# Kernel optimization log

Measured on AMD Instinct MI355X. Metric: run time of the kernel, lower is better.

## Reference

```python
import jax, jax.numpy as jnp
import numpy as np

B, T, S, H, L = 64, 512, 400, 768, 9


def setup_inputs() -> dict:
    rng = np.random.default_rng(0)
    attn = np.zeros((B, T), np.int32)
    ids_lens = np.zeros((B, S), np.int32)
    for bi in range(B):
        Lb = int(rng.integers(T // 2, T + 1))  # valid wordpiece count
        lens = []
        rem = Lb
        while rem > 0 and len(lens) < S - 1:
            l = int(min(rng.integers(1, 4), rem))  # 1-3 wordpieces per word
            lens.append(l)
            rem -= l
        if rem > 0:
            lens.append(rem)
        attn[bi, :Lb] = 1
        ids_lens[bi, :len(lens)] = np.asarray(lens, np.int32)
    label_ids = rng.integers(0, L, (B, S)).astype(np.int32)
    label_mask = ids_lens > 0
    key = jax.random.key(0)
    k1, k2 = jax.random.split(key)
    last_enc_out = jax.random.normal(k1, (B, T, H), jnp.float32)
    W = jax.random.normal(k2, (H, L), jnp.float32) * 0.02
    b = jnp.zeros((L,), jnp.float32)
    return {
        'last_enc_out': last_enc_out, 'W': W, 'b': b,
        'attention_mask': jnp.asarray(attn), 'ids_lens': jnp.asarray(ids_lens),
        'label_ids': jnp.asarray(label_ids), 'label_mask': jnp.asarray(label_mask),
    }


def reference(last_enc_out, W, b, attention_mask, ids_lens, label_ids, label_mask):
    Bv, Tv, Hv = last_enc_out.shape
    Sv = ids_lens.shape[1]
    # position of each valid token among the row's valid tokens
    tok_pos = jnp.cumsum(attention_mask, axis=1) - 1            # [B,T]
    cum = jnp.cumsum(ids_lens, axis=1)                          # [B,S] nondecreasing
    # word index for each token: first w with cum[w] > tok_pos
    word_idx = jax.vmap(lambda c, p: jnp.searchsorted(c, p, side='right'))(cum, tok_pos)
    valid = attention_mask > 0
    seg = jnp.where(valid, jnp.arange(Bv)[:, None] * Sv + word_idx, Bv * Sv)  # dump slot for pad
    sums = jax.ops.segment_sum(last_enc_out.reshape(Bv * Tv, Hv), seg.reshape(Bv * Tv),
                               num_segments=Bv * Sv + 1)[:Bv * Sv]
    counts = jnp.maximum(ids_lens.reshape(Bv * Sv), 1).astype(last_enc_out.dtype)
    means = (sums / counts[:, None]).reshape(Bv, Sv, Hv)
    word_mask = ids_lens > 0
    bert_embed = jnp.where(word_mask[:, :, None], means, jnp.zeros((), last_enc_out.dtype))
    # dropout is identity in eval mode
    logits = bert_embed @ W + b                                 # [B,S,L]
    logp = jax.nn.log_softmax(logits, axis=-1)
    nll = -jnp.take_along_axis(logp, label_ids[..., None].astype(jnp.int32), axis=-1)[..., 0]
    mf = label_mask.astype(logits.dtype)
    loss = jnp.sum(nll * mf) / jnp.sum(mf)                      # CE with ignore_index masking
    output = jnp.argmax(logits, axis=-1)
    return loss, output
```

## Files before the change

### kernel.cpp

```cpp
#include <hip/hip_runtime.h>
#include <math.h>

#define Bdim 64
#define Tdim 512
#define Sdim 400
#define Hdim 768
#define Ldim 9
#define PSTRIDE 12

#define PROJ_BLOCKS 2048
#define ROWS_PER_BLK 16

template <int CTRL>
__device__ __forceinline__ float dpp_add(float x) {
  int y = __builtin_amdgcn_update_dpp(0, __float_as_int(x), CTRL, 0xF, 0xF, false);
  return x + __int_as_float(y);
}
__device__ __forceinline__ float wave_sum63(float x) {
  x = dpp_add<0x111>(x);
  x = dpp_add<0x112>(x);
  x = dpp_add<0x114>(x);
  x = dpp_add<0x118>(x);
  x = dpp_add<0x142>(x);
  x = dpp_add<0x143>(x);
  return x;
}

__global__ __launch_bounds__(192, 4) void proj_kernel(
    const float* __restrict__ enc, const float* __restrict__ W,
    float* __restrict__ proj, float* __restrict__ accum,
    unsigned* __restrict__ counter) {
  int tid = threadIdx.x;
  int lane = tid & 63;
  int w = tid >> 6;
  int l0 = w * 3;
  int base = blockIdx.x * ROWS_PER_BLK;

  if (blockIdx.x == 0) {
    if (tid < 2) accum[tid] = 0.0f;
    if (tid == 2) *counter = 0u;
  }

  float wf[3][4][3];
#pragma unroll
  for (int k = 0; k < 3; ++k)
#pragma unroll
    for (int j = 0; j < 4; ++j) {
      int h = 4 * lane + 256 * k + j;
#pragma unroll
      for (int c = 0; c < 3; ++c) wf[k][j][c] = W[(size_t)h * Ldim + l0 + c];
    }

  const float4* encf4 = (const float4*)enc;

  float4 xa0, xa1, xa2, xb0, xb1, xb2;
#define LDROW(v0, v1, v2, IDX)                                             \
  {                                                                        \
    const float4* r_ = encf4 + (size_t)(base + (IDX)) * (Hdim / 4);        \
    v0 = r_[lane]; v1 = r_[lane + 64]; v2 = r_[lane + 128];                \
  }
#define PROCROW(v0, v1, v2, IDX)                                           \
  {                                                                        \
    float dd[3];                                                           \
    _Pragma("unroll") for (int c = 0; c < 3; ++c) {                        \
      dd[c] = v0.x * wf[0][0][c] + v0.y * wf[0][1][c] +                    \
              v0.z * wf[0][2][c] + v0.w * wf[0][3][c] +                    \
              v1.x * wf[1][0][c] + v1.y * wf[1][1][c] +                    \
              v1.z * wf[1][2][c] + v1.w * wf[1][3][c] +                    \
              v2.x * wf[2][0][c] + v2.y * wf[2][1][c] +                    \
              v2.z * wf[2][2][c] + v2.w * wf[2][3][c];                     \
      dd[c] = wave_sum63(dd[c]);                                           \
    }                                                                      \
    if (lane == 63) {                                                      \
      float* dst = proj + (size_t)(base + (IDX)) * PSTRIDE + l0;           \
      dst[0] = dd[0]; dst[1] = dd[1]; dst[2] = dd[2];                      \
    }                                                                      \
  }

  LDROW(xa0, xa1, xa2, 0)
  LDROW(xb0, xb1, xb2, 1)
#pragma unroll
  for (int i = 0; i < ROWS_PER_BLK; i += 2) {
    PROCROW(xa0, xa1, xa2, i)
    if (i + 2 < ROWS_PER_BLK) LDROW(xa0, xa1, xa2, i + 2)
    PROCROW(xb0, xb1, xb2, i + 1)
    if (i + 3 < ROWS_PER_BLK) LDROW(xb0, xb1, xb2, i + 3)
  }
#undef LDROW
#undef PROCROW
}

__global__ __launch_bounds__(Tdim) void rowword_kernel(
    const float* __restrict__ proj, const float* __restrict__ bias,
    const int* __restrict__ attn, const int* __restrict__ ids_lens,
    const int* __restrict__ label_ids, float* __restrict__ out,
    float* __restrict__ accum, unsigned* __restrict__ counter) {
  int b = blockIdx.x;
  int tid = threadIdx.x;
  int lane = tid & 63, wid = tid >> 6;
  __shared__ int p2t[Tdim];
  __shared__ int wst[Sdim];
  __shared__ int wsum[8];
  __shared__ int totsm;
  __shared__ float ssm[8], csm[8];

  int m = attn[b * Tdim + tid];
  int x = m;
#pragma unroll
  for (int off = 1; off < 64; off <<= 1) {
    int v = __shfl_up(x, off, 64);
    if (lane >= off) x += v;
  }
  if (lane == 63) wsum[wid] = x;
  __syncthreads();
  if (tid < 8) {
    int s = wsum[tid], y = s;
#pragma unroll
    for (int off = 1; off < 8; off <<= 1) {
      int v = __shfl_up(y, off, 64);
      if (tid >= off) y += v;
    }
    wsum[tid] = y - s;
    if (tid == 7) totsm = y;
  }
  __syncthreads();
  x += wsum[wid];
  if (m) p2t[x - 1] = tid;
  int nv_local = totsm;
  __syncthreads();

  int len = (tid < Sdim) ? ids_lens[b * Sdim + tid] : 0;
  int x2 = len;
#pragma unroll
  for (int off = 1; off < 64; off <<= 1) {
    int v = __shfl_up(x2, off, 64);
    if (lane >= off) x2 += v;
  }
  if (lane == 63) wsum[wid] = x2;
  __syncthreads();
  if (tid < 8) {
    int s = wsum[tid], y = s;
#pragma unroll
    for (int off = 1; off < 8; off <<= 1) {
      int v = __shfl_up(y, off, 64);
      if (tid >= off) y += v;
    }
    wsum[tid] = y - s;
  }
  __syncthreads();
  x2 += wsum[wid];
  if (tid < Sdim) wst[tid] = x2 - len;
  __syncthreads();

  float nll = 0.0f, cnt = 0.0f;
  if (tid < Sdim) {
    int bs = b * Sdim + tid;
    float sum[Ldim];
#pragma unroll
    for (int l = 0; l < Ldim; ++l) sum[l] = 0.0f;
    if (len > 0) {
      int start = wst[tid];
      for (int j = 0; j < len; ++j) {
        int q = start + j;
        if (q >= nv_local) break;
        const float* pr = proj + ((size_t)(b << 9) + p2t[q]) * PSTRIDE;
        const float4* pr4 = (const float4*)pr;
        float4 r0 = pr4[0], r1 = pr4[1];
        float r8 = pr[8];
        sum[0] += r0.x; sum[1] += r0.y; sum[2] += r0.z; sum[3] += r0.w;
        sum[4] += r1.x; sum[5] += r1.y; sum[6] += r1.z; sum[7] += r1.w;
        sum[8] += r8;
      }
    }
    float inv = (len > 0) ? 1.0f / (float)len : 0.0f;
    float lg[Ldim];
#pragma unroll
    for (int l = 0; l < Ldim; ++l) lg[l] = sum[l] * inv + bias[l];

    int amax = 0;
    float mx = lg[0];
#pragma unroll
    for (int l = 1; l < Ldim; ++l)
      if (lg[l] > mx) { mx = lg[l]; amax = l; }
    out[1 + bs] = (float)amax;

    if (len > 0) {
      float se = 0.0f;
#pragma unroll
      for (int l = 0; l < Ldim; ++l) se += expf(lg[l] - mx);
      float lse = mx + logf(se);
      int lab = label_ids[bs];
      float ll = lg[0];
#pragma unroll
      for (int l = 1; l < Ldim; ++l) ll = (lab == l) ? lg[l] : ll;
      nll = lse - ll;
      cnt = 1.0f;
    }
  }

#pragma unroll
  for (int off = 32; off > 0; off >>= 1) {
    nll += __shfl_down(nll, off, 64);
    cnt += __shfl_down(cnt, off, 64);
  }
  if (lane == 0) { ssm[wid] = nll; csm[wid] = cnt; }
  __syncthreads();
  if (tid == 0) {
    float S = 0.f, C = 0.f;
#pragma unroll
    for (int k = 0; k < 8; ++k) { S += ssm[k]; C += csm[k]; }
    atomicAdd(&accum[0], S);
    atomicAdd(&accum[1], C);
    __threadfence();
    unsigned prev = atomicAdd(counter, 1u);
    if (prev == gridDim.x - 1) {
      __threadfence();
      float Sf = atomicAdd(&accum[0], 0.0f);
      float Cf = atomicAdd(&accum[1], 0.0f);
      out[0] = Sf / Cf;
    }
  }
}

extern "C" void kernel_launch(void* const* d_in, const int* in_sizes, int n_in,
                              void* d_out, int out_size, void* d_ws, size_t ws_size,
                              hipStream_t stream) {
  const float* enc     = (const float*)d_in[0];
  const float* W       = (const float*)d_in[1];
  const float* bias    = (const float*)d_in[2];
  const int* attn      = (const int*)d_in[3];
  const int* ids_lens  = (const int*)d_in[4];
  const int* label_ids = (const int*)d_in[5];

  float* out = (float*)d_out;

  char* ws = (char*)d_ws;
  size_t off0 = 0;
  float* accum      = (float*)(ws + off0);    off0 += 128;
  unsigned* counter = (unsigned*)(ws + off0); off0 += 128;
  float* proj       = (float*)(ws + off0);    off0 += (size_t)Bdim * Tdim * PSTRIDE * sizeof(float);

  proj_kernel<<<PROJ_BLOCKS, 192, 0, stream>>>(enc, W, proj, accum, counter);
  rowword_kernel<<<Bdim, Tdim, 0, stream>>>(proj, bias, attn, ids_lens,
                                            label_ids, out, accum, counter);
}
```

Baseline: 34.58 us.

## Fuse projection and word pooling per batch quarter, skip padded tokens

Combines the token projection and the per-word pooling/loss into a single kernel that launches four blocks per batch row. Each block compacts the valid tokens, projects only a window of them (its 128-token quarter plus a small overlap) into shared memory, and pools the words that start in that quarter. This removes the global proj buffer round-trip and skips projecting padded tokens. The atomic counter finalisation is replaced by per-block partials and a tiny reduction kernel. In exchange, the grid is only 256 blocks of 512 threads, so the projection has less parallelism than the 2048-block version. Overlap tokens are also projected twice.

```diff
diff --git a/kernel.cpp b/kernel.cpp
--- a/kernel.cpp
+++ b/kernel.cpp
@@ -6,10 +6,9 @@
 #define Sdim 400
 #define Hdim 768
 #define Ldim 9
-#define PSTRIDE 12
-
-#define PROJ_BLOCKS 2048
-#define ROWS_PER_BLK 16
+
+#define QWIN 130
+#define LPROJ_ROWS 132
 
 template <int CTRL>
 __device__ __forceinline__ float dpp_add(float x) {
@@ -26,175 +25,178 @@
   return x;
 }
 
-__global__ __launch_bounds__(192, 4) void proj_kernel(
+__global__ __launch_bounds__(512, 2) void fused_kernel(
     const float* __restrict__ enc, const float* __restrict__ W,
-    float* __restrict__ proj, float* __restrict__ accum,
-    unsigned* __restrict__ counter) {
+    const float* __restrict__ bias, const int* __restrict__ attn,
+    const int* __restrict__ ids_lens, const int* __restrict__ label_ids,
+    float* __restrict__ out, float2* __restrict__ partials) {
+  int blk = blockIdx.x;
+  int b = blk >> 2;
+  int part = blk & 3;
+  int q0 = part << 7;
   int tid = threadIdx.x;
-  int lane = tid & 63;
-  int w = tid >> 6;
-  int l0 = w * 3;
-  int base = blockIdx.x * ROWS_PER_BLK;
-
-  if (blockIdx.x == 0) {
-    if (tid < 2) accum[tid] = 0.0f;
-    if (tid == 2) *counter = 0u;
-  }
-
-  float wf[3][4][3];
-#pragma unroll
-  for (int k = 0; k < 3; ++k)
-#pragma unroll
-    for (int j = 0; j < 4; ++j) {
-      int h = 4 * lane + 256 * k + j;
-#pragma unroll
-      for (int c = 0; c < 3; ++c) wf[k][j][c] = W[(size_t)h * Ldim + l0 + c];
-    }
-
-  const float4* encf4 = (const float4*)enc;
-
-  float4 xa0, xa1, xa2, xb0, xb1, xb2;
-#define LDROW(v0, v1, v2, IDX)                                             \
+  int lane = tid & 63, wid = tid >> 6;
+
+  __shared__ int p2t[Tdim];
+  __shared__ int wst[Sdim];
+  __shared__ float lproj[LPROJ_ROWS][12];
+  __shared__ int wsum[8];
+  __shared__ int totsm;
+  __shared__ float ssm[8], csm[8];
+
+  int m = attn[b * Tdim + tid];
+  int x = m;
+#pragma unroll
+  for (int off = 1; off < 64; off <<= 1) {
+    int v = __shfl_up(x, off, 64);
+    if (lane >= off) x += v;
+  }
+  if (lane == 63) wsum[wid] = x;
+  __syncthreads();
+  if (tid < 8) {
+    int s = wsum[tid], y = s;
+#pragma unroll
+    for (int off = 1; off < 8; off <<= 1) {
+      int v = __shfl_up(y, off, 64);
+      if (tid >= off) y += v;
+    }
+    wsum[tid] = y - s;
+    if (tid == 7) totsm = y;
+  }
+  __syncthreads();
+  x += wsum[wid];
+  if (m) p2t[x - 1] = tid;
+  int nv = totsm;
+  __syncthreads();
+
+  int len = (tid < Sdim) ? ids_lens[b * Sdim + tid] : 0;
+  int x2 = len;
+#pragma unroll
+  for (int off = 1; off < 64; off <<= 1) {
+    int v = __shfl_up(x2, off, 64);
+    if (lane >= off) x2 += v;
+  }
+  if (lane == 63) wsum[wid] = x2;
+  __syncthreads();
+  if (tid < 8) {
+    int s = wsum[tid], y = s;
+#pragma unroll
+    for (int off = 1; off < 8; off <<= 1) {
+      int v = __shfl_up(y, off, 64);
+      if (tid >= off) y += v;
+    }
+    wsum[tid] = y - s;
+  }
+  __syncthreads();
+  x2 += wsum[wid];
+  if (tid < Sdim) wst[tid] = x2 - len;
+  __syncthreads();
+
+  int lim = q0 + QWIN;
+  if (lim > nv) lim = nv;
+  if (wid < 6) {
+    int g = (wid >= 3) ? 1 : 0;
+    int l0 = (wid - 3 * g) * 3;
+    int tc = lim - q0 - g;
+    tc = (tc > 0) ? ((tc + 1) >> 1) : 0;
+
+    if (tc > 0) {
+      float wf[3][4][3];
+#pragma unroll
+      for (int k = 0; k < 3; ++k)
+#pragma unroll
+        for (int j = 0; j < 4; ++j) {
+          int h = 4 * lane + 256 * k + j;
+#pragma unroll
+          for (int c = 0; c < 3; ++c) wf[k][j][c] = W[(size_t)h * Ldim + l0 + c];
+        }
+      const float4* encb = (const float4*)enc + (size_t)(b << 9) * (Hdim / 4);
+
+      float4 A0, A1, A2, B0, B1, B2;
+#define LDK(V0, V1, V2, K)                                                 \
   {                                                                        \
-    const float4* r_ = encf4 + (size_t)(base + (IDX)) * (Hdim / 4);        \
-    v0 = r_[lane]; v1 = r_[lane + 64]; v2 = r_[lane + 128];                \
-  }
-#define PROCROW(v0, v1, v2, IDX)                                           \
+    int t_ = p2t[q0 + g + 2 * (K)];                                        \
+    const float4* r_ = encb + (size_t)t_ * (Hdim / 4);                     \
+    V0 = r_[lane]; V1 = r_[lane + 64]; V2 = r_[lane + 128];                \
+  }
+#define PRK(V0, V1, V2, K)                                                 \
   {                                                                        \
     float dd[3];                                                           \
     _Pragma("unroll") for (int c = 0; c < 3; ++c) {                        \
-      dd[c] = v0.x * wf[0][0][c] + v0.y * wf[0][1][c] +                    \
-              v0.z * wf[0][2][c] + v0.w * wf[0][3][c] +                    \
-              v1.x * wf[1][0][c] + v1.y * wf[1][1][c] +                    \
-              v1.z * wf[1][2][c] + v1.w * wf[1][3][c] +                    \
-              v2.x * wf[2][0][c] + v2.y * wf[2][1][c] +                    \
-              v2.z * wf[2][2][c] + v2.w * wf[2][3][c];                     \
+      dd[c] = V0.x * wf[0][0][c] + V0.y * wf[0][1][c] +                    \
+              V0.z * wf[0][2][c] + V0.w * wf[0][3][c] +                    \
+              V1.x * wf[1][0][c] + V1.y * wf[1][1][c] +                    \
+              V1.z * wf[1][2][c] + V1.w * wf[1][3][c] +                    \
+              V2.x * wf[2][0][c] + V2.y * wf[2][1][c] +                    \
+              V2.z * wf[2][2][c] + V2.w * wf[2][3][c];                     \
       dd[c] = wave_sum63(dd[c]);                                           \
     }                                                                      \
     if (lane == 63) {                                                      \
-      float* dst = proj + (size_t)(base + (IDX)) * PSTRIDE + l0;           \
-      dst[0] = dd[0]; dst[1] = dd[1]; dst[2] = dd[2];                      \
+      int row_ = g + 2 * (K);                                              \
+      lproj[row_][l0 + 0] = dd[0];                                         \
+      lproj[row_][l0 + 1] = dd[1];                                         \
+      lproj[row_][l0 + 2] = dd[2];                                         \
     }                                                                      \
   }
-
-  LDROW(xa0, xa1, xa2, 0)
-  LDROW(xb0, xb1, xb2, 1)
-#pragma unroll
-  for (int i = 0; i < ROWS_PER_BLK; i += 2) {
-    PROCROW(xa0, xa1, xa2, i)
-    if (i + 2 < ROWS_PER_BLK) LDROW(xa0, xa1, xa2, i + 2)
-    PROCROW(xb0, xb1, xb2, i + 1)
-    if (i + 3 < ROWS_PER_BLK) LDROW(xb0, xb1, xb2, i + 3)
-  }
-#undef LDROW
-#undef PROCROW
-}
-
-__global__ __launch_bounds__(Tdim) void rowword_kernel(
-    const float* __restrict__ proj, const float* __restrict__ bias,
-    const int* __restrict__ attn, const int* __restrict__ ids_lens,
-    const int* __restrict__ label_ids, float* __restrict__ out,
-    float* __restrict__ accum, unsigned* __restrict__ counter) {
-  int b = blockIdx.x;
-  int tid = threadIdx.x;
-  int lane = tid & 63, wid = tid >> 6;
-  __shared__ int p2t[Tdim];
-  __shared__ int wst[Sdim];
-  __shared__ int wsum[8];
-  __shared__ int totsm;
-  __shared__ float ssm[8], csm[8];
-
-  int m = attn[b * Tdim + tid];
-  int x = m;
-#pragma unroll
-  for (int off = 1; off < 64; off <<= 1) {
-    int v = __shfl_up(x, off, 64);
-    if (lane >= off) x += v;
-  }
-  if (lane == 63) wsum[wid] = x;
-  __syncthreads();
-  if (tid < 8) {
-    int s = wsum[tid], y = s;
-#pragma unroll
-    for (int off = 1; off < 8; off <<= 1) {
-      int v = __shfl_up(y, off, 64);
-      if (tid >= off) y += v;
-    }
-    wsum[tid] = y - s;
-    if (tid == 7) totsm = y;
-  }
-  __syncthreads();
-  x += wsum[wid];
-  if (m) p2t[x - 1] = tid;
-  int nv_local = totsm;
-  __syncthreads();
-
-  int len = (tid < Sdim) ? ids_lens[b * Sdim + tid] : 0;
-  int x2 = len;
-#pragma unroll
-  for (int off = 1; off < 64; off <<= 1) {
-    int v = __shfl_up(x2, off, 64);
-    if (lane >= off) x2 += v;
-  }
-  if (lane == 63) wsum[wid] = x2;
-  __syncthreads();
-  if (tid < 8) {
-    int s = wsum[tid], y = s;
-#pragma unroll
-    for (int off = 1; off < 8; off <<= 1) {
-      int v = __shfl_up(y, off, 64);
-      if (tid >= off) y += v;
-    }
-    wsum[tid] = y - s;
-  }
-  __syncthreads();
-  x2 += wsum[wid];
-  if (tid < Sdim) wst[tid] = x2 - len;
+      LDK(A0, A1, A2, 0)
+      if (tc > 1) LDK(B0, B1, B2, 1)
+      int k = 0;
+      for (; k + 2 < tc; k += 2) {
+        PRK(A0, A1, A2, k)
+        LDK(A0, A1, A2, k + 2)
+        PRK(B0, B1, B2, k + 1)
+        if (k + 3 < tc) LDK(B0, B1, B2, k + 3)
+      }
+      PRK(A0, A1, A2, k)
+      if (k + 1 < tc) PRK(B0, B1, B2, k + 1)
+#undef LDK
+#undef PRK
+    }
+  }
   __syncthreads();
 
   float nll = 0.0f, cnt = 0.0f;
   if (tid < Sdim) {
-    int bs = b * Sdim + tid;
-    float sum[Ldim];
-#pragma unroll
-    for (int l = 0; l < Ldim; ++l) sum[l] = 0.0f;
-    if (len > 0) {
-      int start = wst[tid];
-      for (int j = 0; j < len; ++j) {
-        int q = start + j;
-        if (q >= nv_local) break;
-        const float* pr = proj + ((size_t)(b << 9) + p2t[q]) * PSTRIDE;
-        const float4* pr4 = (const float4*)pr;
-        float4 r0 = pr4[0], r1 = pr4[1];
-        float r8 = pr[8];
-        sum[0] += r0.x; sum[1] += r0.y; sum[2] += r0.z; sum[3] += r0.w;
-        sum[4] += r1.x; sum[5] += r1.y; sum[6] += r1.z; sum[7] += r1.w;
-        sum[8] += r8;
+    int st = wst[tid];
+    int stc = (st > 511) ? 511 : st;
+    if ((stc >> 7) == part) {
+      int bs = b * Sdim + tid;
+      float sum[Ldim];
+#pragma unroll
+      for (int l = 0; l < Ldim; ++l) sum[l] = 0.0f;
+      if (len > 0) {
+        for (int j = 0; j < len; ++j) {
+          int q = st + j;
+          if (q >= nv) break;
+          const float* pr = lproj[q - q0];
+#pragma unroll
+          for (int l = 0; l < Ldim; ++l) sum[l] += pr[l];
+        }
       }
-    }
-    float inv = (len > 0) ? 1.0f / (float)len : 0.0f;
-    float lg[Ldim];
-#pragma unroll
-    for (int l = 0; l < Ldim; ++l) lg[l] = sum[l] * inv + bias[l];
-
-    int amax = 0;
-    float mx = lg[0];
-#pragma unroll
-    for (int l = 1; l < Ldim; ++l)
-      if (lg[l] > mx) { mx = lg[l]; amax = l; }
-    out[1 + bs] = (float)amax;
-
-    if (len > 0) {
-      float se = 0.0f;
-#pragma unroll
-      for (int l = 0; l < Ldim; ++l) se += expf(lg[l] - mx);
-      float lse = mx + logf(se);
-      int lab = label_ids[bs];
-      float ll = lg[0];
-#pragma unroll
-      for (int l = 1; l < Ldim; ++l) ll = (lab == l) ? lg[l] : ll;
-      nll = lse - ll;
-      cnt = 1.0f;
+      float inv = (len > 0) ? 1.0f / (float)len : 0.0f;
+      float lg[Ldim];
+#pragma unroll
+      for (int l = 0; l < Ldim; ++l) lg[l] = sum[l] * inv + bias[l];
+
+      int amax = 0;
+      float mx = lg[0];
+#pragma unroll
+      for (int l = 1; l < Ldim; ++l)
+        if (lg[l] > mx) { mx = lg[l]; amax = l; }
+      out[1 + bs] = (float)amax;
+
+      if (len > 0) {
+        float se = 0.0f;
+#pragma unroll
+        for (int l = 0; l < Ldim; ++l) se += expf(lg[l] - mx);
+        float lse = mx + logf(se);
+        int lab = label_ids[bs];
+        float ll = lg[0];
+#pragma unroll
+        for (int l = 1; l < Ldim; ++l) ll = (lab == l) ? lg[l] : ll;
+        nll = lse - ll;
+        cnt = 1.0f;
+      }
     }
   }
 
@@ -209,17 +211,27 @@
     float S = 0.f, C = 0.f;
 #pragma unroll
     for (int k = 0; k < 8; ++k) { S += ssm[k]; C += csm[k]; }
-    atomicAdd(&accum[0], S);
-    atomicAdd(&accum[1], C);
-    __threadfence();
-    unsigned prev = atomicAdd(counter, 1u);
-    if (prev == gridDim.x - 1) {
-      __threadfence();
-      float Sf = atomicAdd(&accum[0], 0.0f);
-      float Cf = atomicAdd(&accum[1], 0.0f);
-      out[0] = Sf / Cf;
-    }
-  }
+    float2 pc; pc.x = S; pc.y = C;
+    partials[blk] = pc;
+  }
+}
+
+__global__ __launch_bounds__(256) void final_kernel(
+    const float2* __restrict__ partials, float* __restrict__ out) {
+  int tid = threadIdx.x;
+  float2 pc = partials[tid];
+  float s = pc.x, c = pc.y;
+#pragma unroll
+  for (int off = 32; off > 0; off >>= 1) {
+    s += __shfl_down(s, off, 64);
+    c += __shfl_down(c, off, 64);
+  }
+  __shared__ float ss[4], cc[4];
+  int wid = tid >> 6, lane = tid & 63;
+  if (lane == 0) { ss[wid] = s; cc[wid] = c; }
+  __syncthreads();
+  if (tid == 0)
+    out[0] = (ss[0] + ss[1] + ss[2] + ss[3]) / (cc[0] + cc[1] + cc[2] + cc[3]);
 }
 
 extern "C" void kernel_launch(void* const* d_in, const int* in_sizes, int n_in,
@@ -234,13 +246,9 @@
 
   float* out = (float*)d_out;
 
-  char* ws = (char*)d_ws;
-  size_t off0 = 0;
-  float* accum      = (float*)(ws + off0);    off0 += 128;
-  unsigned* counter = (unsigned*)(ws + off0); off0 += 128;
-  float* proj       = (float*)(ws + off0);    off0 += (size_t)Bdim * Tdim * PSTRIDE * sizeof(float);
-
-  proj_kernel<<<PROJ_BLOCKS, 192, 0, stream>>>(enc, W, proj, accum, counter);
-  rowword_kernel<<<Bdim, Tdim, 0, stream>>>(proj, bias, attn, ids_lens,
-                                            label_ids, out, accum, counter);
-}
+  float2* partials = (float2*)d_ws;
+
+  fused_kernel<<<Bdim * 4, 512, 0, stream>>>(enc, W, bias, attn, ids_lens,
+                                             label_ids, out, partials);
+  final_kernel<<<1, 256, 0, stream>>>(partials, out);
+}
```

Result: faster. 33.00 us (median of 3 runs) (-4.6%).

## Skip padded tokens in projection and compute all labels per wave

Applied to the files above, without the earlier changes.

Each wave now handles 32 consecutive tokens and computes all nine label dot products for each one, instead of three waves each computing three labels for the same row. A ballot over the attention mask finds the count of leading valid tokens, and the wave only loads and projects those, so encoder rows for padding are never read. This is meant to cut the memory traffic of the bandwidth-bound projection. In exchange, each wave keeps more weight values in registers. It also assumes the valid tokens form a contiguous prefix of each row, which holds for these inputs but is not required by the reference.

```diff
diff --git a/kernel.cpp b/kernel.cpp
--- a/kernel.cpp
+++ b/kernel.cpp
@@ -8,8 +8,7 @@
 #define Ldim 9
 #define PSTRIDE 12
 
-#define PROJ_BLOCKS 2048
-#define ROWS_PER_BLK 16
+#define TPW 32
 
 template <int CTRL>
 __device__ __forceinline__ float dpp_add(float x) {
@@ -26,68 +25,77 @@
   return x;
 }
 
-__global__ __launch_bounds__(192, 4) void proj_kernel(
+__global__ __launch_bounds__(256, 2) void proj_kernel(
     const float* __restrict__ enc, const float* __restrict__ W,
-    float* __restrict__ proj, float* __restrict__ accum,
-    unsigned* __restrict__ counter) {
+    const int* __restrict__ attn, float* __restrict__ proj,
+    float* __restrict__ accum, unsigned* __restrict__ counter) {
   int tid = threadIdx.x;
   int lane = tid & 63;
-  int w = tid >> 6;
-  int l0 = w * 3;
-  int base = blockIdx.x * ROWS_PER_BLK;
+  int wv = (blockIdx.x << 2) | (tid >> 6);
+  int t0 = wv * TPW;
 
   if (blockIdx.x == 0) {
     if (tid < 2) accum[tid] = 0.0f;
     if (tid == 2) *counter = 0u;
   }
 
-  float wf[3][4][3];
-#pragma unroll
-  for (int k = 0; k < 3; ++k)
+  int mb = attn[t0 + (lane & 31)];
+  unsigned long long bal = __ballot(mb != 0);
+  unsigned low = (unsigned)bal;
+  unsigned inv = ~low;
+  int vc = inv ? (__ffs(inv) - 1) : 32;
+  if (vc == 0) return;
+
+  float wf[3][4][Ldim];
+#pragma unroll
+  for (int c = 0; c < 3; ++c)
 #pragma unroll
     for (int j = 0; j < 4; ++j) {
-      int h = 4 * lane + 256 * k + j;
-#pragma unroll
-      for (int c = 0; c < 3; ++c) wf[k][j][c] = W[(size_t)h * Ldim + l0 + c];
+      int h = 4 * lane + 256 * c + j;
+#pragma unroll
+      for (int l = 0; l < Ldim; ++l) wf[c][j][l] = W[(size_t)h * Ldim + l];
     }
 
   const float4* encf4 = (const float4*)enc;
 
-  float4 xa0, xa1, xa2, xb0, xb1, xb2;
-#define LDROW(v0, v1, v2, IDX)                                             \
+  float4 A0, A1, A2, B0, B1, B2;
+#define LDT(V0, V1, V2, K)                                                 \
   {                                                                        \
-    const float4* r_ = encf4 + (size_t)(base + (IDX)) * (Hdim / 4);        \
-    v0 = r_[lane]; v1 = r_[lane + 64]; v2 = r_[lane + 128];                \
-  }
-#define PROCROW(v0, v1, v2, IDX)                                           \
+    const float4* r_ = encf4 + (size_t)(t0 + (K)) * (Hdim / 4);            \
+    V0 = r_[lane]; V1 = r_[lane + 64]; V2 = r_[lane + 128];                \
+  }
+#define PRT(V0, V1, V2, K)                                                 \
   {                                                                        \
-    float dd[3];                                                           \
-    _Pragma("unroll") for (int c = 0; c < 3; ++c) {                        \
-      dd[c] = v0.x * wf[0][0][c] + v0.y * wf[0][1][c] +                    \
-              v0.z * wf[0][2][c] + v0.w * wf[0][3][c] +                    \
-              v1.x * wf[1][0][c] + v1.y * wf[1][1][c] +                    \
-              v1.z * wf[1][2][c] + v1.w * wf[1][3][c] +                    \
-              v2.x * wf[2][0][c] + v2.y * wf[2][1][c] +                    \
-              v2.z * wf[2][2][c] + v2.w * wf[2][3][c];                     \
-      dd[c] = wave_sum63(dd[c]);                                           \
+    float dd[Ldim];                                                        \
+    _Pragma("unroll") for (int l = 0; l < Ldim; ++l) {                     \
+      dd[l] = V0.x * wf[0][0][l] + V0.y * wf[0][1][l] +                    \
+              V0.z * wf[0][2][l] + V0.w * wf[0][3][l] +                    \
+              V1.x * wf[1][0][l] + V1.y * wf[1][1][l] +                    \
+              V1.z * wf[1][2][l] + V1.w * wf[1][3][l] +                    \
+              V2.x * wf[2][0][l] + V2.y * wf[2][1][l] +                    \
+              V2.z * wf[2][2][l] + V2.w * wf[2][3][l];                     \
+      dd[l] = wave_sum63(dd[l]);                                           \
     }                                                                      \
     if (lane == 63) {                                                      \
-      float* dst = proj + (size_t)(base + (IDX)) * PSTRIDE + l0;           \
-      dst[0] = dd[0]; dst[1] = dd[1]; dst[2] = dd[2];                      \
+      float* dst = proj + (size_t)(t0 + (K)) * PSTRIDE;                    \
+      *(float4*)(dst) = make_float4(dd[0], dd[1], dd[2], dd[3]);           \
+      *(float4*)(dst + 4) = make_float4(dd[4], dd[5], dd[6], dd[7]);       \
+      dst[8] = dd[8];                                                      \
     }                                                                      \
   }
 
-  LDROW(xa0, xa1, xa2, 0)
-  LDROW(xb0, xb1, xb2, 1)
-#pragma unroll
-  for (int i = 0; i < ROWS_PER_BLK; i += 2) {
-    PROCROW(xa0, xa1, xa2, i)
-    if (i + 2 < ROWS_PER_BLK) LDROW(xa0, xa1, xa2, i + 2)
-    PROCROW(xb0, xb1, xb2, i + 1)
-    if (i + 3 < ROWS_PER_BLK) LDROW(xb0, xb1, xb2, i + 3)
-  }
-#undef LDROW
-#undef PROCROW
+  LDT(A0, A1, A2, 0)
+  int k = 0;
+  while (true) {
+    if (k + 1 < vc) LDT(B0, B1, B2, k + 1)
+    PRT(A0, A1, A2, k)
+    if (++k >= vc) break;
+    if (k + 1 < vc) LDT(A0, A1, A2, k + 1)
+    PRT(B0, B1, B2, k)
+    if (++k >= vc) break;
+  }
+#undef LDT
+#undef PRT
 }
 
 __global__ __launch_bounds__(Tdim) void rowword_kernel(
@@ -240,7 +248,8 @@
   unsigned* counter = (unsigned*)(ws + off0); off0 += 128;
   float* proj       = (float*)(ws + off0);    off0 += (size_t)Bdim * Tdim * PSTRIDE * sizeof(float);
 
-  proj_kernel<<<PROJ_BLOCKS, 192, 0, stream>>>(enc, W, proj, accum, counter);
+  int nwaves = (Bdim * Tdim) / TPW;
+  proj_kernel<<<nwaves / 4, 256, 0, stream>>>(enc, W, attn, proj, accum, counter);
   rowword_kernel<<<Bdim, Tdim, 0, stream>>>(proj, bias, attn, ids_lens,
                                             label_ids, out, accum, counter);
 }
```

Result: faster. 33.01 us (-4.5%).
